# Kernel optimization log

Measured on AMD Instinct MI355X. Metric: run time of the kernel, lower is better.

## Reference

```python
import jax, jax.numpy as jnp
import numpy as np

BOUND = 1.2


def _ste_sign(v, bound):
    # forward: sign(v); backward: d clamp(v,-bound,bound)/dv (straight-through estimator)
    clipped = jnp.clip(v, -bound, bound)
    return jax.lax.stop_gradient(jnp.sign(v) - clipped) + clipped


def setup_inputs() -> dict:
    key = jax.random.key(0)
    kx, kw = jax.random.split(key)
    x = jax.random.normal(kx, (32, 128, 112, 112), dtype=jnp.float32)
    # xavier_normal_ with gain=2.0: std = gain * sqrt(2/(fan_in+fan_out)), fan = C*k*k
    fan = 128 * 3 * 3
    std = 2.0 * np.sqrt(2.0 / (fan + fan))
    weights = jax.random.normal(kw, (128, 128, 3, 3), dtype=jnp.float32) * std
    return {"x": x, "weights": weights}


def reference(x, weights):
    # Binarize activations and weights with STE (training-mode math of BConv)
    xb = _ste_sign(x, BOUND)
    wb = _ste_sign(weights, BOUND)
    # conv2d, NCHW input, OIHW weights, stride 1, padding 1, dilation 1
    out = jax.lax.conv_general_dilated(
        xb, wb,
        window_strides=(1, 1),
        padding=((1, 1), (1, 1)),
        lhs_dilation=(1, 1),
        rhs_dilation=(1, 1),
        dimension_numbers=("NCHW", "OIHW", "NCHW"),
        feature_group_count=1,
    )
    return out
```

## Files before the change

kernel.cpp:

```cpp
#include <hip/hip_runtime.h>
#include <cstdint>
#include <cstddef>

#define NIMG 32
#define C    128
#define OC   128
#define HW   112
#define HWSZ (HW * HW)
#define NTAP 9
#define PHW  114
#define XROW (PHW * C)
#define XIMG (PHW * XROW)
#define XQ_BYTES ((size_t)NIMG * XIMG)
#define AWQ_BYTES ((size_t)4 * 9 * 4 * 64 * 16)

typedef int v4i  __attribute__((ext_vector_type(4)));
typedef int v16i __attribute__((ext_vector_type(16)));

__device__ __forceinline__ uint32_t sign_byte(uint32_t bits) {
    return ((bits >> 31) * 0xFEu) ^ 1u;
}

__global__ void fill_border(uint8_t* __restrict__ xq) {
    int tid = blockIdx.x * blockDim.x + threadIdx.x;
    int n = tid / 3616, u = tid % 3616;
    size_t off;
    if (u < 912)        off = (size_t)u * 16;
    else if (u < 1824)  off = (size_t)113 * XROW + (size_t)(u - 912) * 16;
    else {
        int j = u - 1824;
        int r = (j >> 4) + 1;
        int side = (j >> 3) & 1;
        int cu = j & 7;
        off = (size_t)r * XROW + (size_t)side * (113 * C) + (size_t)cu * 16;
    }
    *(uint4*)(xq + (size_t)n * XIMG + off) = make_uint4(0u, 0u, 0u, 0u);
}

__global__ __launch_bounds__(256) void pack_x_cl(const float* __restrict__ x,
                                                 uint8_t* __restrict__ xq) {
    __shared__ __align__(16) uint8_t slds[2 * 112 * 144];
    int n = blockIdx.x / 56, hp = blockIdx.x % 56;
    int h0 = hp * 2;

    int task = threadIdx.x;
    if (task < 224) {
        int r = task / 112, rem = task % 112;
        int word = rem / 28, pxg = rem % 28;
        const float* xp = x + ((size_t)(n * C + word * 32)) * HWSZ
                            + (size_t)(h0 + r) * HW + pxg * 4;
        uint32_t dw[4][8];
        #pragma unroll
        for (int i = 0; i < 8; ++i) {
            uint32_t a0 = 0, a1 = 0, a2 = 0, a3 = 0;
            #pragma unroll
            for (int b = 0; b < 4; ++b) {
                float4 v = *reinterpret_cast<const float4*>(xp + (size_t)(i * 4 + b) * HWSZ);
                a0 |= sign_byte(__float_as_uint(v.x)) << (8 * b);
                a1 |= sign_byte(__float_as_uint(v.y)) << (8 * b);
                a2 |= sign_byte(__float_as_uint(v.z)) << (8 * b);
                a3 |= sign_byte(__float_as_uint(v.w)) << (8 * b);
            }
            dw[0][i] = a0; dw[1][i] = a1; dw[2][i] = a2; dw[3][i] = a3;
        }
        #pragma unroll
        for (int j = 0; j < 4; ++j) {
            uint8_t* sp = &slds[(size_t)((r * 112) + pxg * 4 + j) * 144 + word * 32];
            *(uint4*)sp        = make_uint4(dw[j][0], dw[j][1], dw[j][2], dw[j][3]);
            *(uint4*)(sp + 16) = make_uint4(dw[j][4], dw[j][5], dw[j][6], dw[j][7]);
        }
    }
    __syncthreads();

    uint8_t* dst = xq + (size_t)n * XIMG + (size_t)(h0 + 1) * XROW + C;
    #pragma unroll
    for (int rep = 0; rep < 7; ++rep) {
        int u = threadIdx.x + rep * 256;
        int row = u / 896, i = u % 896;
        *(uint4*)(dst + (size_t)row * XROW + (size_t)i * 16) =
            *(const uint4*)&slds[(size_t)(row * 112 + (i >> 3)) * 144 + (i & 7) * 16];
    }
}

__global__ void pack_w_frag(const float* __restrict__ w, uint32_t* __restrict__ awq) {
    int tid = blockIdx.x * blockDim.x + threadIdx.x;
    int d = tid & 3, l = (tid >> 2) & 63, f = tid >> 8;
    int ks = f & 3, tf = f >> 2;
    int tap = tf % 9, wv = tf / 9;
    int o = wv * 32 + (l & 31);
    int cb = ks * 32 + ((l >> 5) & 1) * 16 + d * 4;
    uint32_t acc = 0;
    #pragma unroll
    for (int jj = 0; jj < 4; ++jj) {
        uint32_t bits = __float_as_uint(w[(size_t)(o * C + cb + jj) * NTAP + tap]);
        acc |= sign_byte(bits) << (8 * jj);
    }
    awq[tid] = acc;
}

__global__ __launch_bounds__(256, 2) void bconv_mfma(const uint8_t* __restrict__ xq,
                                                     const uint8_t* __restrict__ awq,
                                                     float* __restrict__ out) {
    __shared__ __align__(16) uint8_t sxq[4 * XROW];
    int bid = blockIdx.x;
    int swz = (bid & 7) * 224 + (bid >> 3);
    int n = swz / 56, hp = swz % 56;
    int h0 = hp * 2;

    const uint8_t* src = xq + (size_t)n * XIMG + (size_t)h0 * XROW;
    #pragma unroll
    for (int rep = 0; rep < 15; ++rep) {
        int u = threadIdx.x + rep * 256;
        if (u < 3648) {
            int pix = (u >> 3) % PHW;
            uint4 v = *(const uint4*)(src + (size_t)u * 16);
            int a = (u * 16) ^ ((pix & 7) << 4);
            *(uint4*)&sxq[a] = v;
        }
    }

    int wv = threadIdx.x >> 6, l = threadIdx.x & 63;
    int l31 = l & 31, lk = (l >> 5) * 16;

    v4i A[9][4];
    #pragma unroll
    for (int tap = 0; tap < 9; ++tap)
        #pragma unroll
        for (int ks = 0; ks < 4; ++ks) {
            int f = (wv * 9 + tap) * 4 + ks;
            A[tap][ks] = *(const v4i*)(awq + (size_t)f * 1024 + (size_t)l * 16);
        }
    __syncthreads();

    float* outb = out + ((size_t)n * OC + wv * 32) * HWSZ + (size_t)h0 * HW;

    for (int nt = 0; nt < 7; ++nt) {
        int p = nt * 32 + l31;
        int rl = (p >= HW) ? 1 : 0;
        int w = p - rl * HW;

        int ad[3][4];
        #pragma unroll
        for (int kw = 0; kw < 3; ++kw) {
            int col = w + kw;
            int x4 = (col & 7) << 4;
            int b0 = rl * XROW + col * C;
            #pragma unroll
            for (int ks = 0; ks < 4; ++ks)
                ad[kw][ks] = b0 + ((ks * 32 + lk) ^ x4);
        }

        v16i acc = {0,0,0,0,0,0,0,0,0,0,0,0,0,0,0,0};
        #pragma unroll
        for (int kh = 0; kh < 3; ++kh)
            #pragma unroll
            for (int kw = 0; kw < 3; ++kw)
                #pragma unroll
                for (int ks = 0; ks < 4; ++ks) {
                    v4i b = *(const v4i*)&sxq[kh * XROW + ad[kw][ks]];
                    acc = __builtin_amdgcn_mfma_i32_32x32x32_i8(
                              A[kh * 3 + kw][ks], b, acc, 0, 0, 0);
                }

        #pragma unroll
        for (int r = 0; r < 16; ++r) {
            int oof = (r & 3) + 8 * (r >> 2) + 4 * (l >> 5);
            outb[(size_t)oof * HWSZ + rl * HW + w] = (float)acc[r];
        }
    }
}

extern "C" void kernel_launch(void* const* d_in, const int* in_sizes, int n_in,
                              void* d_out, int out_size, void* d_ws, size_t ws_size,
                              hipStream_t stream) {
    const float* x   = (const float*)d_in[0];
    const float* wts = (const float*)d_in[1];
    float* out = (float*)d_out;
    uint8_t* ws = (uint8_t*)d_ws;

    uint8_t*  xq  = ws;
    uint32_t* awq = (uint32_t*)(ws + XQ_BYTES);

    hipLaunchKernelGGL(fill_border, dim3(NIMG * 3616 / 256), dim3(256), 0, stream, xq);
    hipLaunchKernelGGL(pack_w_frag, dim3(144), dim3(256), 0, stream, wts, awq);
    hipLaunchKernelGGL(pack_x_cl, dim3(NIMG * 56), dim3(256), 0, stream, x, xq);
    hipLaunchKernelGGL(bconv_mfma, dim3(NIMG * 56), dim3(256), 0, stream,
                       xq, (const uint8_t*)awq, out);
}
```

Baseline: 141.9 us.

## Fuse activation binarization and packing into the conv kernel, dropping intermediate buffer

```diff
diff --git a/kernel.cpp b/kernel.cpp
--- a/kernel.cpp
+++ b/kernel.cpp
@@ -10,77 +10,10 @@
 #define NTAP 9
 #define PHW  114
 #define XROW (PHW * C)
-#define XIMG (PHW * XROW)
-#define XQ_BYTES ((size_t)NIMG * XIMG)
 #define AWQ_BYTES ((size_t)4 * 9 * 4 * 64 * 16)
 
 typedef int v4i  __attribute__((ext_vector_type(4)));
 typedef int v16i __attribute__((ext_vector_type(16)));
-
-__device__ __forceinline__ uint32_t sign_byte(uint32_t bits) {
-    return ((bits >> 31) * 0xFEu) ^ 1u;
-}
-
-__global__ void fill_border(uint8_t* __restrict__ xq) {
-    int tid = blockIdx.x * blockDim.x + threadIdx.x;
-    int n = tid / 3616, u = tid % 3616;
-    size_t off;
-    if (u < 912)        off = (size_t)u * 16;
-    else if (u < 1824)  off = (size_t)113 * XROW + (size_t)(u - 912) * 16;
-    else {
-        int j = u - 1824;
-        int r = (j >> 4) + 1;
-        int side = (j >> 3) & 1;
-        int cu = j & 7;
-        off = (size_t)r * XROW + (size_t)side * (113 * C) + (size_t)cu * 16;
-    }
-    *(uint4*)(xq + (size_t)n * XIMG + off) = make_uint4(0u, 0u, 0u, 0u);
-}
-
-__global__ __launch_bounds__(256) void pack_x_cl(const float* __restrict__ x,
-                                                 uint8_t* __restrict__ xq) {
-    __shared__ __align__(16) uint8_t slds[2 * 112 * 144];
-    int n = blockIdx.x / 56, hp = blockIdx.x % 56;
-    int h0 = hp * 2;
-
-    int task = threadIdx.x;
-    if (task < 224) {
-        int r = task / 112, rem = task % 112;
-        int word = rem / 28, pxg = rem % 28;
-        const float* xp = x + ((size_t)(n * C + word * 32)) * HWSZ
-                            + (size_t)(h0 + r) * HW + pxg * 4;
-        uint32_t dw[4][8];
-        #pragma unroll
-        for (int i = 0; i < 8; ++i) {
-            uint32_t a0 = 0, a1 = 0, a2 = 0, a3 = 0;
-            #pragma unroll
-            for (int b = 0; b < 4; ++b) {
-                float4 v = *reinterpret_cast<const float4*>(xp + (size_t)(i * 4 + b) * HWSZ);
-                a0 |= sign_byte(__float_as_uint(v.x)) << (8 * b);
-                a1 |= sign_byte(__float_as_uint(v.y)) << (8 * b);
-                a2 |= sign_byte(__float_as_uint(v.z)) << (8 * b);
-                a3 |= sign_byte(__float_as_uint(v.w)) << (8 * b);
-            }
-            dw[0][i] = a0; dw[1][i] = a1; dw[2][i] = a2; dw[3][i] = a3;
-        }
-        #pragma unroll
-        for (int j = 0; j < 4; ++j) {
-            uint8_t* sp = &slds[(size_t)((r * 112) + pxg * 4 + j) * 144 + word * 32];
-            *(uint4*)sp        = make_uint4(dw[j][0], dw[j][1], dw[j][2], dw[j][3]);
-            *(uint4*)(sp + 16) = make_uint4(dw[j][4], dw[j][5], dw[j][6], dw[j][7]);
-        }
-    }
-    __syncthreads();
-
-    uint8_t* dst = xq + (size_t)n * XIMG + (size_t)(h0 + 1) * XROW + C;
-    #pragma unroll
-    for (int rep = 0; rep < 7; ++rep) {
-        int u = threadIdx.x + rep * 256;
-        int row = u / 896, i = u % 896;
-        *(uint4*)(dst + (size_t)row * XROW + (size_t)i * 16) =
-            *(const uint4*)&slds[(size_t)(row * 112 + (i >> 3)) * 144 + (i & 7) * 16];
-    }
-}
 
 __global__ void pack_w_frag(const float* __restrict__ w, uint32_t* __restrict__ awq) {
     int tid = blockIdx.x * blockDim.x + threadIdx.x;
@@ -93,35 +26,88 @@
     #pragma unroll
     for (int jj = 0; jj < 4; ++jj) {
         uint32_t bits = __float_as_uint(w[(size_t)(o * C + cb + jj) * NTAP + tap]);
-        acc |= sign_byte(bits) << (8 * jj);
+        acc |= (((bits >> 31) * 0xFEu) ^ 1u) << (8 * jj);
     }
     awq[tid] = acc;
 }
 
-__global__ __launch_bounds__(256, 2) void bconv_mfma(const uint8_t* __restrict__ xq,
-                                                     const uint8_t* __restrict__ awq,
-                                                     float* __restrict__ out) {
+__global__ __launch_bounds__(256, 2) void bconv_fused(const float* __restrict__ x,
+                                                      const uint8_t* __restrict__ awq,
+                                                      float* __restrict__ out) {
     __shared__ __align__(16) uint8_t sxq[4 * XROW];
     int bid = blockIdx.x;
     int swz = (bid & 7) * 224 + (bid >> 3);
     int n = swz / 56, hp = swz % 56;
     int h0 = hp * 2;
 
-    const uint8_t* src = xq + (size_t)n * XIMG + (size_t)h0 * XROW;
     #pragma unroll
-    for (int rep = 0; rep < 15; ++rep) {
-        int u = threadIdx.x + rep * 256;
-        if (u < 3648) {
-            int pix = (u >> 3) % PHW;
-            uint4 v = *(const uint4*)(src + (size_t)u * 16);
-            int a = (u * 16) ^ ((pix & 7) << 4);
-            *(uint4*)&sxq[a] = v;
+    for (int rep = 0; rep < 2; ++rep) {
+        int task = threadIdx.x + rep * 256;
+        if (task < 448) {
+            int r = task / 112;
+            int rem = task % 112;
+            int word = rem / 28, pxg = rem % 28;
+            int hr = h0 - 1 + r;
+            int col0 = 1 + pxg * 4;
+            int sbase = r * XROW;
+            if (hr >= 0 && hr < HW) {
+                const float* xp = x + ((size_t)(n * C + word * 32)) * HWSZ
+                                    + (size_t)hr * HW + pxg * 4;
+                uint32_t dw[4][8];
+                #pragma unroll
+                for (int j = 0; j < 4; ++j)
+                    #pragma unroll
+                    for (int d = 0; d < 8; ++d) dw[j][d] = 0u;
+                #pragma unroll
+                for (int c = 0; c < 32; ++c) {
+                    float4 v = *reinterpret_cast<const float4*>(xp + (size_t)c * HWSZ);
+                    uint32_t bm = 0xFFu << (8 * (c & 3));
+                    int d = c >> 2;
+                    dw[0][d] |= ((uint32_t)((int)__float_as_uint(v.x) >> 31)) & bm;
+                    dw[1][d] |= ((uint32_t)((int)__float_as_uint(v.y) >> 31)) & bm;
+                    dw[2][d] |= ((uint32_t)((int)__float_as_uint(v.z) >> 31)) & bm;
+                    dw[3][d] |= ((uint32_t)((int)__float_as_uint(v.w) >> 31)) & bm;
+                }
+                #pragma unroll
+                for (int j = 0; j < 4; ++j) {
+                    int col = col0 + j;
+                    int cb = col * 128 + word * 32;
+                    int sw = (col & 7) << 4;
+                    uint32_t d0 = (dw[j][0] & 0xFEFEFEFEu) ^ 0x01010101u;
+                    uint32_t d1 = (dw[j][1] & 0xFEFEFEFEu) ^ 0x01010101u;
+                    uint32_t d2 = (dw[j][2] & 0xFEFEFEFEu) ^ 0x01010101u;
+                    uint32_t d3 = (dw[j][3] & 0xFEFEFEFEu) ^ 0x01010101u;
+                    *(uint4*)&sxq[sbase + (cb ^ sw)] = make_uint4(d0, d1, d2, d3);
+                    uint32_t d4 = (dw[j][4] & 0xFEFEFEFEu) ^ 0x01010101u;
+                    uint32_t d5 = (dw[j][5] & 0xFEFEFEFEu) ^ 0x01010101u;
+                    uint32_t d6 = (dw[j][6] & 0xFEFEFEFEu) ^ 0x01010101u;
+                    uint32_t d7 = (dw[j][7] & 0xFEFEFEFEu) ^ 0x01010101u;
+                    *(uint4*)&sxq[sbase + ((cb + 16) ^ sw)] = make_uint4(d4, d5, d6, d7);
+                }
+            } else {
+                #pragma unroll
+                for (int j = 0; j < 4; ++j) {
+                    int col = col0 + j;
+                    int cb = col * 128 + word * 32;
+                    int sw = (col & 7) << 4;
+                    *(uint4*)&sxq[sbase + (cb ^ sw)]        = make_uint4(0u, 0u, 0u, 0u);
+                    *(uint4*)&sxq[sbase + ((cb + 16) ^ sw)] = make_uint4(0u, 0u, 0u, 0u);
+                }
+            }
+        } else if (task < 456) {
+            int j = task - 448;
+            int r = j >> 1, side = j & 1;
+            int col = side ? 113 : 0;
+            int sw = (col & 7) << 4;
+            #pragma unroll
+            for (int k = 0; k < 8; ++k)
+                *(uint4*)&sxq[r * XROW + ((col * 128 + k * 16) ^ sw)] =
+                    make_uint4(0u, 0u, 0u, 0u);
         }
     }
 
     int wv = threadIdx.x >> 6, l = threadIdx.x & 63;
     int l31 = l & 31, lk = (l >> 5) * 16;
-
     v4i A[9][4];
     #pragma unroll
     for (int tap = 0; tap < 9; ++tap)
@@ -176,14 +162,9 @@
     const float* x   = (const float*)d_in[0];
     const float* wts = (const float*)d_in[1];
     float* out = (float*)d_out;
-    uint8_t* ws = (uint8_t*)d_ws;
+    uint32_t* awq = (uint32_t*)d_ws;
 
-    uint8_t*  xq  = ws;
-    uint32_t* awq = (uint32_t*)(ws + XQ_BYTES);
-
-    hipLaunchKernelGGL(fill_border, dim3(NIMG * 3616 / 256), dim3(256), 0, stream, xq);
     hipLaunchKernelGGL(pack_w_frag, dim3(144), dim3(256), 0, stream, wts, awq);
-    hipLaunchKernelGGL(pack_x_cl, dim3(NIMG * 56), dim3(256), 0, stream, x, xq);
-    hipLaunchKernelGGL(bconv_mfma, dim3(NIMG * 56), dim3(256), 0, stream,
-                       xq, (const uint8_t*)awq, out);
+    hipLaunchKernelGGL(bconv_fused, dim3(NIMG * 56), dim3(256), 0, stream,
+                       x, (const uint8_t*)awq, out);
 }
```

Measured after the change: 126.6 us. -10.8%, faster.
